# Kernel tuning notes

Measured on AMD Instinct MI355X. Metric: run time of the kernel, lower is better.

The kernel has to match this reference:

```python
import jax, jax.numpy as jnp
import numpy as np

PAD_ID = 2


def _positional_encoding(seq_len, d_model, dtype):
    # pe[pos, i] = cos((pos+1)/10000**(i/d))      if i even
    #            = sin((pos+1)/10000**((i+1)/d))  if i odd
    i = jnp.arange(d_model)
    even = (i % 2) == 0
    exponent = jnp.where(even, i, i + 1).astype(jnp.float32) / d_model
    inv_div = 10000.0 ** (-exponent)                      # [d]
    pos = (jnp.arange(seq_len) + 1).astype(jnp.float32)   # [S]
    angle = pos[:, None] * inv_div[None, :]               # [S, d]
    pe = jnp.where(even[None, :], jnp.cos(angle), jnp.sin(angle))
    return pe.astype(dtype)


def setup_inputs() -> dict:
    key = jax.random.key(0)
    k1, k2, k3 = jax.random.split(key, 3)
    d_model, vocab = 1024, 32000
    x = jax.random.randint(k1, (8, 2048), 0, vocab, dtype=jnp.int32)
    weight = jax.random.normal(k2, (d_model, vocab), dtype=jnp.float32) * 0.02
    bias = jax.random.normal(k3, (d_model,), dtype=jnp.float32) * 0.02
    return {"x": x, "weight": weight, "bias": bias}


def reference(x, weight, bias):
    # one_hot(x) @ weight.T + bias  ==  gather columns of weight
    emb = jnp.take(weight.T, x, axis=0) + bias            # [B, S, d]
    B, S, d = emb.shape
    pe = _positional_encoding(S, d, emb.dtype)            # [S, d]
    emb = emb + pe[None, :, :]
    # input_mask[b, i, j] = (x[b, j] == PAD_ID), broadcast over rows i
    pad = (x == PAD_ID)                                   # [B, S]
    input_mask = jnp.broadcast_to(pad[:, None, :], (B, S, S))
    return emb, input_mask
```

## Files before the change

kernel.cpp:

```cpp
#include <hip/hip_runtime.h>
#include <math.h>

#define D_MODEL 1024
#define SEQ     2048
#define BATCH   8
#define VOCAB   32000
#define PAD_ID  2

typedef float f32x4 __attribute__((ext_vector_type(4)));

#define INV_EXP_C (13.287712379549449f / 1024.0f)

__global__ __launch_bounds__(256) void pe_kernel(float* __restrict__ pe) {
    const int s  = blockIdx.x;
    const int d0 = threadIdx.x * 4;
    const float pos = (float)(s + 1);

    const float inv0 = exp2f(-(float)(d0)     * INV_EXP_C);
    const float inv1 = exp2f(-(float)(d0 + 2) * INV_EXP_C);
    const float inv2 = exp2f(-(float)(d0 + 4) * INV_EXP_C);

    float s1, c1;
    sincosf(pos * inv1, &s1, &c1);

    f32x4 v;
    v.x = cosf(pos * inv0);
    v.y = s1;
    v.z = c1;
    v.w = sinf(pos * inv2);

    *(f32x4*)(pe + (size_t)s * D_MODEL + d0) = v;
}

__global__ __launch_bounds__(256) void transpose_bias_kernel(
        const float* __restrict__ w,
        const float* __restrict__ bias,
        float*       __restrict__ wT) {
    __shared__ float tile[64][65];
    const int v0 = blockIdx.x * 64;
    const int d0 = blockIdx.y * 64;

    {
        const int vx = (threadIdx.x & 15) * 4;
        const int dy = threadIdx.x >> 4;
        #pragma unroll
        for (int i = 0; i < 64; i += 16) {
            const int d = d0 + dy + i;
            const f32x4 val = *(const f32x4*)(w + (size_t)d * VOCAB + v0 + vx);
            const float bv = bias[d];
            tile[dy + i][vx + 0] = val.x + bv;
            tile[dy + i][vx + 1] = val.y + bv;
            tile[dy + i][vx + 2] = val.z + bv;
            tile[dy + i][vx + 3] = val.w + bv;
        }
    }
    __syncthreads();
    {
        const int dx = (threadIdx.x & 15) * 4;
        const int vy = threadIdx.x >> 4;
        #pragma unroll
        for (int i = 0; i < 64; i += 16) {
            f32x4 o;
            o.x = tile[dx + 0][vy + i];
            o.y = tile[dx + 1][vy + i];
            o.z = tile[dx + 2][vy + i];
            o.w = tile[dx + 3][vy + i];
            *(f32x4*)(wT + (size_t)(v0 + vy + i) * D_MODEL + d0 + dx) = o;
        }
    }
}

template <int MODE>
__global__ __launch_bounds__(256) void emb_mask_kernel(
        const int*   __restrict__ x,
        const float* __restrict__ w,
        const float* __restrict__ bias,
        const float* __restrict__ pe,
        float*       __restrict__ emb,
        float*       __restrict__ mask) {
    const int s = blockIdx.x;
    const int b = blockIdx.y;
    const int t = threadIdx.x;

    const int tok = x[b * SEQ + s];
    const int d0 = t * 4;

    f32x4 wv;
    if (MODE == 0) {
        wv = *(const f32x4*)(w + (size_t)tok * D_MODEL + d0);
    } else {
        const float* wc = w + tok;
        const f32x4 bv = *(const f32x4*)(bias + d0);
        wv.x = wc[(size_t)(d0 + 0) * VOCAB] + bv.x;
        wv.y = wc[(size_t)(d0 + 1) * VOCAB] + bv.y;
        wv.z = wc[(size_t)(d0 + 2) * VOCAB] + bv.z;
        wv.w = wc[(size_t)(d0 + 3) * VOCAB] + bv.w;
    }

    f32x4 pv;
    if (MODE == 2) {
        const float pos  = (float)(s + 1);
        const float inv0 = exp2f(-(float)(d0)     * INV_EXP_C);
        const float inv1 = exp2f(-(float)(d0 + 2) * INV_EXP_C);
        const float inv2 = exp2f(-(float)(d0 + 4) * INV_EXP_C);
        float s1, c1;
        sincosf(pos * inv1, &s1, &c1);
        pv.x = cosf(pos * inv0);
        pv.y = s1;
        pv.z = c1;
        pv.w = sinf(pos * inv2);
    } else {
        pv = *(const f32x4*)(pe + (size_t)s * D_MODEL + d0);
    }

    f32x4 o;
    o.x = wv.x + pv.x;
    o.y = wv.y + pv.y;
    o.z = wv.z + pv.z;
    o.w = wv.w + pv.w;

    f32x4* eptr = (f32x4*)(emb + ((size_t)(b * SEQ + s)) * D_MODEL + d0);
    __builtin_nontemporal_store(o, eptr);

    const int j0 = t * 8;
    const int4 xi0 = *(const int4*)(x + b * SEQ + j0);
    const int4 xi1 = *(const int4*)(x + b * SEQ + j0 + 4);

    f32x4 m0, m1;
    m0.x = (xi0.x == PAD_ID) ? 1.0f : 0.0f;
    m0.y = (xi0.y == PAD_ID) ? 1.0f : 0.0f;
    m0.z = (xi0.z == PAD_ID) ? 1.0f : 0.0f;
    m0.w = (xi0.w == PAD_ID) ? 1.0f : 0.0f;
    m1.x = (xi1.x == PAD_ID) ? 1.0f : 0.0f;
    m1.y = (xi1.y == PAD_ID) ? 1.0f : 0.0f;
    m1.z = (xi1.z == PAD_ID) ? 1.0f : 0.0f;
    m1.w = (xi1.w == PAD_ID) ? 1.0f : 0.0f;

    float* mrow = mask + ((size_t)b * SEQ + s) * SEQ + j0;
    __builtin_nontemporal_store(m0, (f32x4*)mrow);
    __builtin_nontemporal_store(m1, (f32x4*)(mrow + 4));
}

extern "C" void kernel_launch(void* const* d_in, const int* in_sizes, int n_in,
                              void* d_out, int out_size, void* d_ws, size_t ws_size,
                              hipStream_t stream) {
    const int*   x    = (const int*)d_in[0];
    const float* w    = (const float*)d_in[1];
    const float* bias = (const float*)d_in[2];

    float* emb  = (float*)d_out;
    float* mask = (float*)d_out + (size_t)BATCH * SEQ * D_MODEL;

    const size_t wt_floats = (size_t)VOCAB * D_MODEL;
    const size_t pe_floats = (size_t)SEQ * D_MODEL;
    const size_t need_full = (wt_floats + pe_floats) * sizeof(float);
    const size_t need_pe   = pe_floats * sizeof(float);

    dim3 grid(SEQ, BATCH);
    dim3 block(256);

    if (ws_size >= need_full) {
        float* wT = (float*)d_ws;
        float* pe = (float*)d_ws + wt_floats;
        pe_kernel<<<dim3(SEQ), block, 0, stream>>>(pe);
        transpose_bias_kernel<<<dim3(VOCAB / 64, D_MODEL / 64), block, 0, stream>>>(w, bias, wT);
        emb_mask_kernel<0><<<grid, block, 0, stream>>>(x, wT, bias, pe, emb, mask);
    } else if (ws_size >= need_pe) {
        float* pe = (float*)d_ws;
        pe_kernel<<<dim3(SEQ), block, 0, stream>>>(pe);
        emb_mask_kernel<1><<<grid, block, 0, stream>>>(x, w, bias, pe, emb, mask);
    } else {
        emb_mask_kernel<2><<<grid, block, 0, stream>>>(x, w, bias, nullptr, emb, mask);
    }
}
```

Baseline: 332.0 us.

## Replace full weight transpose with token bucketing and fused tile-wise scatter

Drops the full transposed copy of the weight matrix in workspace. Tokens are instead bucketed by vocab id using count, scan and scatter kernels, and a fused kernel transposes each 64x64 weight tile in shared memory and writes embedding rows directly for the tokens that use those vocab entries. This removes the 131MB write and reread of the transposed weight. In exchange it adds several small serial kernels, including a single-block scan, plus atomics and uncoalesced idx reads. The mask is moved to its own kernel.

```diff
diff --git a/kernel.cpp b/kernel.cpp
--- a/kernel.cpp
+++ b/kernel.cpp
@@ -6,6 +6,7 @@
 #define BATCH   8
 #define VOCAB   32000
 #define PAD_ID  2
+#define NTOK    (BATCH * SEQ)
 
 typedef float f32x4 __attribute__((ext_vector_type(4)));
 
@@ -32,97 +33,126 @@
     *(f32x4*)(pe + (size_t)s * D_MODEL + d0) = v;
 }
 
-__global__ __launch_bounds__(256) void transpose_bias_kernel(
+__global__ __launch_bounds__(256) void zero_kernel(int* __restrict__ p, int n) {
+    const int i = blockIdx.x * 256 + threadIdx.x;
+    if (i < n) p[i] = 0;
+}
+
+__global__ __launch_bounds__(256) void count_kernel(const int* __restrict__ x,
+                                                    int* __restrict__ cnt) {
+    const int i = blockIdx.x * 256 + threadIdx.x;
+    atomicAdd(&cnt[x[i]], 1);
+}
+
+__device__ inline int wave_incl_scan(int v) {
+    const int lane = threadIdx.x & 63;
+    #pragma unroll
+    for (int s = 1; s < 64; s <<= 1) {
+        int y = __shfl_up(v, s, 64);
+        if (lane >= s) v += y;
+    }
+    return v;
+}
+
+__global__ __launch_bounds__(1024) void scan_kernel(const int* __restrict__ cnt,
+                                                    int* __restrict__ off,
+                                                    int* __restrict__ cur) {
+    __shared__ int wsum[16];
+    const int t = threadIdx.x, w = t >> 6;
+    int carry = 0;
+    for (int base = 0; base < VOCAB; base += 1024) {
+        const int in = base + t;
+        int v = (in < VOCAB) ? cnt[in] : 0;
+        int inc = wave_incl_scan(v);
+        if ((t & 63) == 63) wsum[w] = inc;
+        __syncthreads();
+        int woff = 0, total = 0;
+        #pragma unroll
+        for (int k = 0; k < 16; ++k) {
+            int s = wsum[k];
+            if (k < w) woff += s;
+            total += s;
+        }
+        __syncthreads();
+        const int excl = carry + woff + inc - v;
+        if (in < VOCAB) { off[in] = excl; cur[in] = excl; }
+        carry += total;
+    }
+    if (t == 0) off[VOCAB] = carry;
+}
+
+__global__ __launch_bounds__(256) void scatter_kernel(const int* __restrict__ x,
+                                                      int* __restrict__ cur,
+                                                      int* __restrict__ idx) {
+    const int i = blockIdx.x * 256 + threadIdx.x;
+    const int p = atomicAdd(&cur[x[i]], 1);
+    idx[p] = i;
+}
+
+__global__ __launch_bounds__(256) void fused_emb_kernel(
         const float* __restrict__ w,
         const float* __restrict__ bias,
-        float*       __restrict__ wT) {
+        const float* __restrict__ pe,
+        const int*   __restrict__ off,
+        const int*   __restrict__ idx,
+        float*       __restrict__ emb) {
     __shared__ float tile[64][65];
     const int v0 = blockIdx.x * 64;
     const int d0 = blockIdx.y * 64;
+    const int t  = threadIdx.x;
 
     {
-        const int vx = (threadIdx.x & 15) * 4;
-        const int dy = threadIdx.x >> 4;
+        const int vx = (t & 15) * 4;
+        const int dy = t >> 4;
         #pragma unroll
         for (int i = 0; i < 64; i += 16) {
             const int d = d0 + dy + i;
             const f32x4 val = *(const f32x4*)(w + (size_t)d * VOCAB + v0 + vx);
             const float bv = bias[d];
-            tile[dy + i][vx + 0] = val.x + bv;
-            tile[dy + i][vx + 1] = val.y + bv;
-            tile[dy + i][vx + 2] = val.z + bv;
-            tile[dy + i][vx + 3] = val.w + bv;
+            tile[vx + 0][dy + i] = val.x + bv;
+            tile[vx + 1][dy + i] = val.y + bv;
+            tile[vx + 2][dy + i] = val.z + bv;
+            tile[vx + 3][dy + i] = val.w + bv;
         }
     }
     __syncthreads();
-    {
-        const int dx = (threadIdx.x & 15) * 4;
-        const int vy = threadIdx.x >> 4;
+
+    const int vl    = t >> 2;
+    const int lane4 = t & 3;
+    const int v     = v0 + vl;
+    const int beg   = off[v];
+    const int end   = off[v + 1];
+
+    for (int k = beg; k < end; ++k) {
+        const int i = idx[k];
+        const int s = i & (SEQ - 1);
+        float* ebase = emb + (size_t)i * D_MODEL + d0;
+        const float* pbase = pe + (size_t)s * D_MODEL + d0;
         #pragma unroll
-        for (int i = 0; i < 64; i += 16) {
+        for (int j = 0; j < 4; ++j) {
+            const int dl = lane4 * 4 + j * 16;
+            f32x4 wv;
+            wv.x = tile[vl][dl + 0];
+            wv.y = tile[vl][dl + 1];
+            wv.z = tile[vl][dl + 2];
+            wv.w = tile[vl][dl + 3];
+            const f32x4 pv = *(const f32x4*)(pbase + dl);
             f32x4 o;
-            o.x = tile[dx + 0][vy + i];
-            o.y = tile[dx + 1][vy + i];
-            o.z = tile[dx + 2][vy + i];
-            o.w = tile[dx + 3][vy + i];
-            *(f32x4*)(wT + (size_t)(v0 + vy + i) * D_MODEL + d0 + dx) = o;
+            o.x = wv.x + pv.x;
+            o.y = wv.y + pv.y;
+            o.z = wv.z + pv.z;
+            o.w = wv.w + pv.w;
+            __builtin_nontemporal_store(o, (f32x4*)(ebase + dl));
         }
     }
 }
 
-template <int MODE>
-__global__ __launch_bounds__(256) void emb_mask_kernel(
-        const int*   __restrict__ x,
-        const float* __restrict__ w,
-        const float* __restrict__ bias,
-        const float* __restrict__ pe,
-        float*       __restrict__ emb,
-        float*       __restrict__ mask) {
+__global__ __launch_bounds__(256) void mask_kernel(const int* __restrict__ x,
+                                                   float* __restrict__ mask) {
     const int s = blockIdx.x;
     const int b = blockIdx.y;
-    const int t = threadIdx.x;
-
-    const int tok = x[b * SEQ + s];
-    const int d0 = t * 4;
-
-    f32x4 wv;
-    if (MODE == 0) {
-        wv = *(const f32x4*)(w + (size_t)tok * D_MODEL + d0);
-    } else {
-        const float* wc = w + tok;
-        const f32x4 bv = *(const f32x4*)(bias + d0);
-        wv.x = wc[(size_t)(d0 + 0) * VOCAB] + bv.x;
-        wv.y = wc[(size_t)(d0 + 1) * VOCAB] + bv.y;
-        wv.z = wc[(size_t)(d0 + 2) * VOCAB] + bv.z;
-        wv.w = wc[(size_t)(d0 + 3) * VOCAB] + bv.w;
-    }
-
-    f32x4 pv;
-    if (MODE == 2) {
-        const float pos  = (float)(s + 1);
-        const float inv0 = exp2f(-(float)(d0)     * INV_EXP_C);
-        const float inv1 = exp2f(-(float)(d0 + 2) * INV_EXP_C);
-        const float inv2 = exp2f(-(float)(d0 + 4) * INV_EXP_C);
-        float s1, c1;
-        sincosf(pos * inv1, &s1, &c1);
-        pv.x = cosf(pos * inv0);
-        pv.y = s1;
-        pv.z = c1;
-        pv.w = sinf(pos * inv2);
-    } else {
-        pv = *(const f32x4*)(pe + (size_t)s * D_MODEL + d0);
-    }
-
-    f32x4 o;
-    o.x = wv.x + pv.x;
-    o.y = wv.y + pv.y;
-    o.z = wv.z + pv.z;
-    o.w = wv.w + pv.w;
-
-    f32x4* eptr = (f32x4*)(emb + ((size_t)(b * SEQ + s)) * D_MODEL + d0);
-    __builtin_nontemporal_store(o, eptr);
-
-    const int j0 = t * 8;
+    const int j0 = threadIdx.x * 8;
+
     const int4 xi0 = *(const int4*)(x + b * SEQ + j0);
     const int4 xi1 = *(const int4*)(x + b * SEQ + j0 + 4);
 
@@ -141,6 +171,47 @@
     __builtin_nontemporal_store(m1, (f32x4*)(mrow + 4));
 }
 
+__global__ __launch_bounds__(256) void fallback_kernel(
+        const int* __restrict__ x, const float* __restrict__ w,
+        const float* __restrict__ bias, float* __restrict__ emb,
+        float* __restrict__ mask) {
+    const int s = blockIdx.x, b = blockIdx.y, t = threadIdx.x;
+    const int tok = x[b * SEQ + s];
+    const int d0 = t * 4;
+
+    const float* wc = w + tok;
+    const f32x4 bv = *(const f32x4*)(bias + d0);
+    const float pos  = (float)(s + 1);
+    const float inv0 = exp2f(-(float)(d0)     * INV_EXP_C);
+    const float inv1 = exp2f(-(float)(d0 + 2) * INV_EXP_C);
+    const float inv2 = exp2f(-(float)(d0 + 4) * INV_EXP_C);
+    float s1, c1;
+    sincosf(pos * inv1, &s1, &c1);
+
+    f32x4 o;
+    o.x = wc[(size_t)(d0 + 0) * VOCAB] + bv.x + cosf(pos * inv0);
+    o.y = wc[(size_t)(d0 + 1) * VOCAB] + bv.y + s1;
+    o.z = wc[(size_t)(d0 + 2) * VOCAB] + bv.z + c1;
+    o.w = wc[(size_t)(d0 + 3) * VOCAB] + bv.w + sinf(pos * inv2);
+    __builtin_nontemporal_store(o, (f32x4*)(emb + ((size_t)(b * SEQ + s)) * D_MODEL + d0));
+
+    const int j0 = t * 8;
+    const int4 xi0 = *(const int4*)(x + b * SEQ + j0);
+    const int4 xi1 = *(const int4*)(x + b * SEQ + j0 + 4);
+    f32x4 m0, m1;
+    m0.x = (xi0.x == PAD_ID) ? 1.0f : 0.0f;
+    m0.y = (xi0.y == PAD_ID) ? 1.0f : 0.0f;
+    m0.z = (xi0.z == PAD_ID) ? 1.0f : 0.0f;
+    m0.w = (xi0.w == PAD_ID) ? 1.0f : 0.0f;
+    m1.x = (xi1.x == PAD_ID) ? 1.0f : 0.0f;
+    m1.y = (xi1.y == PAD_ID) ? 1.0f : 0.0f;
+    m1.z = (xi1.z == PAD_ID) ? 1.0f : 0.0f;
+    m1.w = (xi1.w == PAD_ID) ? 1.0f : 0.0f;
+    float* mrow = mask + ((size_t)b * SEQ + s) * SEQ + j0;
+    __builtin_nontemporal_store(m0, (f32x4*)mrow);
+    __builtin_nontemporal_store(m1, (f32x4*)(mrow + 4));
+}
+
 extern "C" void kernel_launch(void* const* d_in, const int* in_sizes, int n_in,
                               void* d_out, int out_size, void* d_ws, size_t ws_size,
                               hipStream_t stream) {
@@ -151,25 +222,31 @@
     float* emb  = (float*)d_out;
     float* mask = (float*)d_out + (size_t)BATCH * SEQ * D_MODEL;
 
-    const size_t wt_floats = (size_t)VOCAB * D_MODEL;
-    const size_t pe_floats = (size_t)SEQ * D_MODEL;
-    const size_t need_full = (wt_floats + pe_floats) * sizeof(float);
-    const size_t need_pe   = pe_floats * sizeof(float);
-
-    dim3 grid(SEQ, BATCH);
+    const size_t pe_f   = (size_t)SEQ * D_MODEL;
+    const size_t cnt_o  = pe_f;
+    const size_t off_o  = cnt_o + VOCAB;
+    const size_t cur_o  = off_o + VOCAB + 1;
+    const size_t idx_o  = cur_o + VOCAB;
+    const size_t need   = (idx_o + NTOK) * 4;
+
     dim3 block(256);
 
-    if (ws_size >= need_full) {
-        float* wT = (float*)d_ws;
-        float* pe = (float*)d_ws + wt_floats;
+    if (ws_size >= need) {
+        float* pe  = (float*)d_ws;
+        int*   cnt = (int*)d_ws + cnt_o;
+        int*   off = (int*)d_ws + off_o;
+        int*   cur = (int*)d_ws + cur_o;
+        int*   idx = (int*)d_ws + idx_o;
+
         pe_kernel<<<dim3(SEQ), block, 0, stream>>>(pe);
-        transpose_bias_kernel<<<dim3(VOCAB / 64, D_MODEL / 64), block, 0, stream>>>(w, bias, wT);
-        emb_mask_kernel<0><<<grid, block, 0, stream>>>(x, wT, bias, pe, emb, mask);
-    } else if (ws_size >= need_pe) {
-        float* pe = (float*)d_ws;
-        pe_kernel<<<dim3(SEQ), block, 0, stream>>>(pe);
-        emb_mask_kernel<1><<<grid, block, 0, stream>>>(x, w, bias, pe, emb, mask);
+        zero_kernel<<<dim3((VOCAB + 255) / 256), block, 0, stream>>>(cnt, VOCAB);
+        count_kernel<<<dim3(NTOK / 256), block, 0, stream>>>(x, cnt);
+        scan_kernel<<<dim3(1), dim3(1024), 0, stream>>>(cnt, off, cur);
+        scatter_kernel<<<dim3(NTOK / 256), block, 0, stream>>>(x, cur, idx);
+        fused_emb_kernel<<<dim3(VOCAB / 64, D_MODEL / 64), block, 0, stream>>>(
+            w, bias, pe, off, idx, emb);
+        mask_kernel<<<dim3(SEQ, BATCH), block, 0, stream>>>(x, mask);
     } else {
-        emb_mask_kernel<2><<<grid, block, 0, stream>>>(x, w, bias, nullptr, emb, mask);
-    }
-}
+        fallback_kernel<<<dim3(SEQ, BATCH), block, 0, stream>>>(x, w, bias, emb, mask);
+    }
+}
```

After: 375.7 us. 1.13x slower.
